# Performance work log

Hardware: AMD Instinct MI355X
Metric: run time of the kernel (lower is better)

## Reference

```python
import jax, jax.numpy as jnp
import numpy as np

N_CODES = 4096
DIM = 1280
N_TOKENS = 32768


def _l2norm(v, axis=-1, eps=1e-12):
    return v / jnp.maximum(jnp.linalg.norm(v, axis=axis, keepdims=True), eps)


def setup_inputs() -> dict:
    key = jax.random.key(0)
    kx, ke = jax.random.split(key)
    # inputs are L2-normalized vectors per the module's docstring
    x = _l2norm(jax.random.normal(kx, (N_TOKENS, DIM), dtype=jnp.float32))
    # codebook init: uniform(-1/n_codes, 1/n_codes) then L2-normalized (as in __init__)
    embed = jax.random.uniform(ke, (N_CODES, DIM), dtype=jnp.float32,
                               minval=-1.0 / N_CODES, maxval=1.0 / N_CODES)
    embed = _l2norm(embed)
    return {"x": x, "embed": embed}


def reference(x, embed):
    x_sq = jnp.sum(x * x, axis=1, keepdims=True)            # (N, 1)
    e_sq = jnp.sum(embed * embed, axis=1)[None, :]          # (1, K)
    dist = -(x_sq - 2.0 * (x @ embed.T) + e_sq)             # (N, K)
    indices = jnp.argmax(dist, axis=-1)                     # (N,)
    quantized = embed[indices]                              # gather (N, D)
    commit_loss = jnp.mean((x - quantized) ** 2)
    # straight-through estimator
    quantized_ste = x + jax.lax.stop_gradient(quantized - x)
    return quantized_ste, indices, commit_loss
```

## Files before the change

### kernel.cpp

```cpp
#include <hip/hip_runtime.h>
#include <hip/hip_bf16.h>

typedef int i32x4 __attribute__((ext_vector_type(4)));

#define N_TOKENS 32768
#define N_CODES 4096
#define DIM 1280
#define NT 20
#define BUFSZ 24576
#define NBUF 3

__device__ __forceinline__ void load_lds16(const void* g, void* l) {
    __builtin_amdgcn_global_load_lds(
        (const __attribute__((address_space(1))) unsigned int*)g,
        (__attribute__((address_space(3))) unsigned int*)l,
        16, 0, 0);
}

__global__ __launch_bounds__(256) void quantize_i8_kernel(
    const float* __restrict__ X, const float* __restrict__ E,
    signed char* __restrict__ Xq, signed char* __restrict__ Eq,
    float* __restrict__ sxs, float* __restrict__ ses)
{
    int row = blockIdx.x * 4 + (threadIdx.x >> 6);
    const float* src;
    signed char* dst;
    float* scale;
    if (row < N_TOKENS) {
        src = X + (size_t)row * DIM; dst = Xq + (size_t)row * DIM; scale = sxs + row;
    } else {
        int r = row - N_TOKENS;
        if (r >= N_CODES) return;
        src = E + (size_t)r * DIM; dst = Eq + (size_t)r * DIM; scale = ses + r;
    }
    int lane = threadIdx.x & 63;
    const float4* s4 = (const float4*)src;
    float4 v[5];
    float amax = 0.f;
    #pragma unroll
    for (int j = 0; j < 5; ++j) {
        v[j] = s4[j * 64 + lane];
        amax = fmaxf(amax, fmaxf(fmaxf(fabsf(v[j].x), fabsf(v[j].y)),
                                 fmaxf(fabsf(v[j].z), fabsf(v[j].w))));
    }
    #pragma unroll
    for (int d = 1; d < 64; d <<= 1) amax = fmaxf(amax, __shfl_xor(amax, d));
    amax = fmaxf(amax, 1e-20f);
    float inv = 127.0f / amax;
    int* d4 = (int*)dst;
    #pragma unroll
    for (int j = 0; j < 5; ++j) {
        int q0 = (int)rintf(v[j].x * inv), q1 = (int)rintf(v[j].y * inv);
        int q2 = (int)rintf(v[j].z * inv), q3 = (int)rintf(v[j].w * inv);
        d4[j * 64 + lane] = (q0 & 0xFF) | ((q1 & 0xFF) << 8) |
                            ((q2 & 0xFF) << 16) | ((q3 & 0xFF) << 24);
    }
    if (lane == 0) *scale = amax * (1.0f / 127.0f);
}

__global__ __launch_bounds__(512, 4) void gemm_argmax_kernel(
    const signed char* __restrict__ Xq, const signed char* __restrict__ Eq,
    const float* __restrict__ sx, const float* __restrict__ se,
    unsigned* __restrict__ pkeys)
{
    __shared__ __align__(16) char lds[NBUF * BUFSZ];

    int bid = blockIdx.x;
    int swz = (bid & 7) * 512 + (bid >> 3);
    int cb = swz >> 8, rb = swz & 255;
    int row0 = rb << 7, col0 = cb << 8;

    int tid = threadIdx.x;
    int wid = tid >> 6, lane = tid & 63;
    int wm = wid >> 2, wn = wid & 3;
    int lr = lane & 15, g = lane >> 4;

    int slot = (((lr & 1) << 2) + g) ^ ((lr >> 1) & 7);
    int aoff = ((wm << 5) + (lr >> 1)) * 128 + slot * 16;
    int boff = 8192 + ((wn << 5) + (lr >> 1)) * 128 + slot * 16;

    i32x4 acc[4][4] = {};

    auto STAGE = [&](int t) {
        int base = (t % NBUF) * BUFSZ;
        int k0 = t << 6;
        {
            int rp = tid >> 3, c = tid & 7;
            int cp = c ^ (rp & 7);
            int gr = (rp << 1) + (cp >> 2);
            int kc = k0 + ((cp & 3) << 4);
            load_lds16(Xq + (size_t)(row0 + gr) * DIM + kc, lds + base + (tid << 4));
        }
        #pragma unroll
        for (int i = 0; i < 2; ++i) {
            int f = tid + (i << 9);
            int rp = f >> 3, c = f & 7;
            int cp = c ^ (rp & 7);
            int gr = (rp << 1) + (cp >> 2);
            int kc = k0 + ((cp & 3) << 4);
            load_lds16(Eq + (size_t)(col0 + gr) * DIM + kc, lds + base + 8192 + (f << 4));
        }
    };

    auto COMPUTE = [&](int t) {
        int base = (t % NBUF) * BUFSZ;
        const char* pA = lds + base + aoff;
        const char* pB = lds + base + boff;
        i32x4 a[4], b[4];
        #pragma unroll
        for (int m = 0; m < 4; ++m) a[m] = *(const i32x4*)(pA + (m << 10));
        #pragma unroll
        for (int n = 0; n < 4; ++n) b[n] = *(const i32x4*)(pB + (n << 10));
        __builtin_amdgcn_s_setprio(1);
        #pragma unroll
        for (int m = 0; m < 4; ++m)
            #pragma unroll
            for (int n = 0; n < 4; ++n)
                acc[m][n] = __builtin_amdgcn_mfma_i32_16x16x64_i8(
                    a[m], b[n], acc[m][n], 0, 0, 0);
        __builtin_amdgcn_s_setprio(0);
    };

    STAGE(0); STAGE(1);
    asm volatile("s_waitcnt vmcnt(3)" ::: "memory");
    __builtin_amdgcn_s_barrier();
    __builtin_amdgcn_sched_barrier(0);

    for (int t = 0; t < NT - 2; ++t) {
        STAGE(t + 2);
        COMPUTE(t);
        asm volatile("s_waitcnt vmcnt(3)" ::: "memory");
        __builtin_amdgcn_s_barrier();
        __builtin_amdgcn_sched_barrier(0);
    }
    COMPUTE(NT - 2);
    asm volatile("s_waitcnt vmcnt(0)" ::: "memory");
    __builtin_amdgcn_s_barrier();
    __builtin_amdgcn_sched_barrier(0);
    COMPUTE(NT - 1);
    __syncthreads();

    float se_l[4];
    #pragma unroll
    for (int n = 0; n < 4; ++n)
        se_l[n] = se[col0 + (wn << 6) + (n << 4) + lr];

    uint2* lk2 = (uint2*)lds;
    #pragma unroll
    for (int m = 0; m < 4; ++m) {
        #pragma unroll
        for (int r = 0; r < 4; ++r) {
            int row = (wm << 6) + (m << 4) + (g << 2) + r;
            float fx = sx[row0 + row];
            unsigned b1 = 0, b2 = 0;
            #pragma unroll
            for (int n = 0; n < 4; ++n) {
                float s = (float)acc[m][n][r] * (fx * se_l[n]);
                int cib = ((wn & 1) << 6) + (n << 4) + lr;
                unsigned u = __float_as_uint(s);
                u = (u & 0x80000000u) ? ~u : (u | 0x80000000u);
                unsigned key = (u & 0xFFFFFF80u) | (unsigned)(127 - cib);
                if (key > b1) { b2 = b1; b1 = key; }
                else if (key > b2) b2 = key;
            }
            #pragma unroll
            for (int d = 1; d < 16; d <<= 1) {
                unsigned o1 = __shfl_xor(b1, d), o2 = __shfl_xor(b2, d);
                if (o1 > b1) { b2 = (b1 > o2) ? b1 : o2; b1 = o1; }
                else if (o1 > b2) b2 = o1;
            }
            if (lr == 0) {
                uint2 v; v.x = b1; v.y = b2;
                lk2[(row << 2) + wn] = v;
            }
        }
    }
    __syncthreads();
    if (tid < 256) {
        int row = tid >> 1, h = tid & 1;
        uint2 p0 = lk2[(row << 2) + (h << 1)];
        uint2 p1 = lk2[(row << 2) + (h << 1) + 1];
        unsigned b1 = p0.x, b2 = p0.y;
        if (p1.x > b1) { b2 = (b1 > p1.y) ? b1 : p1.y; b1 = p1.x; }
        else if (p1.x > b2) b2 = p1.x;
        uint2 out; out.x = b1; out.y = b2;
        *(uint2*)&pkeys[((size_t)(row0 + row) << 6) + (((cb << 1) + h) << 1)] = out;
    }
}

__global__ __launch_bounds__(64) void refine_gather_kernel(
    const float* __restrict__ X, const float* __restrict__ E,
    const unsigned* __restrict__ pkeys, float* __restrict__ outq,
    float* __restrict__ outidx, float* __restrict__ sums)
{
    int token = blockIdx.x;
    int lane = threadIdx.x;
    unsigned k = pkeys[((size_t)token << 6) + lane];
    unsigned m = k & 0xFFFFFF80u;
    float s = __uint_as_float((m & 0x80000000u) ? (m & 0x7FFFFFFFu) : ~m);
    float smax = s;
    #pragma unroll
    for (int d = 1; d < 64; d <<= 1) smax = fmaxf(smax, __shfl_xor(smax, d));
    bool cand = s >= smax - 3e-3f;
    unsigned long long ball = __ballot(cand);

    const float4* x4 = (const float4*)(X + (size_t)token * DIM);
    float4 xv[5];
    #pragma unroll
    for (int j = 0; j < 5; ++j) xv[j] = x4[j * 64 + lane];

    double best_s = -1.0e300;
    int best_i = 0x7FFFFFFF;
    while (ball) {
        int src = __ffsll(ball) - 1;
        ball &= ball - 1;
        unsigned ck = __shfl(k, src);
        int cidx = ((src >> 1) << 7) + (127 - (int)(ck & 127u));
        const float4* e4 = (const float4*)(E + (size_t)cidx * DIM);
        double d = 0.0, ee = 0.0;
        #pragma unroll
        for (int j = 0; j < 5; ++j) {
            float4 ev = e4[j * 64 + lane];
            d += (double)xv[j].x * (double)ev.x + (double)xv[j].y * (double)ev.y
               + (double)xv[j].z * (double)ev.z + (double)xv[j].w * (double)ev.w;
            ee += (double)ev.x * (double)ev.x + (double)ev.y * (double)ev.y
                + (double)ev.z * (double)ev.z + (double)ev.w * (double)ev.w;
        }
        #pragma unroll
        for (int dd = 1; dd < 64; dd <<= 1) {
            d += __shfl_xor(d, dd);
            ee += __shfl_xor(ee, dd);
        }
        double sc = 2.0 * d - ee;
        if (sc > best_s || (sc == best_s && cidx < best_i)) { best_s = sc; best_i = cidx; }
    }

    const float4* e4 = (const float4*)(E + (size_t)best_i * DIM);
    float4* o4 = (float4*)(outq + (size_t)token * DIM);
    float local = 0.0f;
    #pragma unroll
    for (int j = 0; j < 5; ++j) {
        float4 q = e4[j * 64 + lane];
        o4[j * 64 + lane] = q;
        float dx = xv[j].x - q.x, dy = xv[j].y - q.y;
        float dz = xv[j].z - q.z, dw = xv[j].w - q.w;
        local += dx * dx + dy * dy + dz * dz + dw * dw;
    }
    #pragma unroll
    for (int d = 1; d < 64; d <<= 1) local += __shfl_xor(local, d);
    if (lane == 0) {
        sums[token] = local;
        outidx[token] = (float)best_i;
    }
}

__global__ __launch_bounds__(256) void loss_kernel(
    const float* __restrict__ sums, float* __restrict__ out_loss)
{
    __shared__ double red[256];
    int t = threadIdx.x;
    double s = 0.0;
    for (int i = t; i < N_TOKENS; i += 256) s += (double)sums[i];
    red[t] = s;
    __syncthreads();
    for (int off = 128; off > 0; off >>= 1) {
        if (t < off) red[t] += red[t + off];
        __syncthreads();
    }
    if (t == 0) out_loss[0] = (float)(red[0] / (double)((size_t)N_TOKENS * DIM));
}

extern "C" void kernel_launch(void* const* d_in, const int* in_sizes, int n_in,
                              void* d_out, int out_size, void* d_ws, size_t ws_size,
                              hipStream_t stream)
{
    const float* X = (const float*)d_in[0];
    const float* E = (const float*)d_in[1];

    float* outq = (float*)d_out;
    float* outidx = outq + (size_t)N_TOKENS * DIM;
    float* outloss = outidx + N_TOKENS;

    signed char* Xq = (signed char*)d_out;
    signed char* Eq = Xq + (size_t)N_TOKENS * DIM;
    float* sxs = (float*)(Eq + (size_t)N_CODES * DIM);
    float* ses = sxs + N_TOKENS;

    unsigned* pkeys = (unsigned*)d_ws;
    float* sums = (float*)((char*)d_ws + (size_t)N_TOKENS * 64 * sizeof(unsigned));

    quantize_i8_kernel<<<dim3((N_TOKENS + N_CODES) / 4), dim3(256), 0, stream>>>(
        X, E, Xq, Eq, sxs, ses);
    gemm_argmax_kernel<<<dim3(4096), dim3(512), 0, stream>>>(Xq, Eq, sxs, ses, pkeys);
    refine_gather_kernel<<<dim3(N_TOKENS), dim3(64), 0, stream>>>(X, E, pkeys, outq, outidx, sums);
    loss_kernel<<<dim3(1), dim3(256), 0, stream>>>(sums, outloss);
}
```

Baseline: 380.5 us.

## Enlarge GEMM tile to 256x256 with 128-deep K double-buffered LDS pipeline

The int8 GEMM+argmax kernel moves from 128x256 tiles with a 3-stage 64-deep K pipeline to 256x256 tiles that use 128-deep K stages in two 64KB LDS buffers. Staging loads are interleaved across four MFMA phases per iteration, and the A/B tiles get a new 64-byte row swizzle. The larger tile doubles per-wave accumulators to 8x4 and halves global/LDS traffic per MFMA. In exchange, occupancy drops to 2 blocks per CU, register pressure rises, and the grid is halved to 2048 blocks.

```diff
diff --git a/kernel.cpp b/kernel.cpp
--- a/kernel.cpp
+++ b/kernel.cpp
@@ -6,9 +6,7 @@
 #define N_TOKENS 32768
 #define N_CODES 4096
 #define DIM 1280
-#define NT 20
-#define BUFSZ 24576
-#define NBUF 3
+#define NT 10
 
 __device__ __forceinline__ void load_lds16(const void* g, void* l) {
     __builtin_amdgcn_global_load_lds(
@@ -58,86 +56,93 @@
     if (lane == 0) *scale = amax * (1.0f / 127.0f);
 }
 
-__global__ __launch_bounds__(512, 4) void gemm_argmax_kernel(
+__global__ __launch_bounds__(512, 2) void gemm_argmax_kernel(
     const signed char* __restrict__ Xq, const signed char* __restrict__ Eq,
     const float* __restrict__ sx, const float* __restrict__ se,
     unsigned* __restrict__ pkeys)
 {
-    __shared__ __align__(16) char lds[NBUF * BUFSZ];
+    __shared__ __align__(16) char lds[131072];
 
     int bid = blockIdx.x;
-    int swz = (bid & 7) * 512 + (bid >> 3);
-    int cb = swz >> 8, rb = swz & 255;
-    int row0 = rb << 7, col0 = cb << 8;
+    int swz = (bid & 7) * 256 + (bid >> 3);
+    int cb0 = swz >> 7, rb = swz & 127;
+    int row0 = rb << 8, col0 = cb0 << 8;
 
     int tid = threadIdx.x;
     int wid = tid >> 6, lane = tid & 63;
     int wm = wid >> 2, wn = wid & 3;
     int lr = lane & 15, g = lane >> 4;
 
-    int slot = (((lr & 1) << 2) + g) ^ ((lr >> 1) & 7);
-    int aoff = ((wm << 5) + (lr >> 1)) * 128 + slot * 16;
-    int boff = 8192 + ((wn << 5) + (lr >> 1)) * 128 + slot * 16;
-
-    i32x4 acc[4][4] = {};
-
-    auto STAGE = [&](int t) {
-        int base = (t % NBUF) * BUFSZ;
-        int k0 = t << 6;
-        {
-            int rp = tid >> 3, c = tid & 7;
-            int cp = c ^ (rp & 7);
-            int gr = (rp << 1) + (cp >> 2);
-            int kc = k0 + ((cp & 3) << 4);
-            load_lds16(Xq + (size_t)(row0 + gr) * DIM + kc, lds + base + (tid << 4));
-        }
-        #pragma unroll
-        for (int i = 0; i < 2; ++i) {
-            int f = tid + (i << 9);
-            int rp = f >> 3, c = f & 7;
-            int cp = c ^ (rp & 7);
-            int gr = (rp << 1) + (cp >> 2);
-            int kc = k0 + ((cp & 3) << 4);
-            load_lds16(Eq + (size_t)(col0 + gr) * DIM + kc, lds + base + 8192 + (f << 4));
+    int chunk = g ^ ((lr >> 1) & 3);
+    int aoff = ((wm << 7) + lr) * 64 + (chunk << 4);
+    int boff = 32768 + ((wn << 6) + lr) * 64 + (chunk << 4);
+
+    int f0 = tid, f1 = tid + 512;
+    int cp0 = ((f0 & 3) ^ ((f0 >> 3) & 3)) << 4;
+    int cp1 = ((f1 & 3) ^ ((f1 >> 3) & 3)) << 4;
+    const signed char* sA0 = Xq + (size_t)(row0 + (f0 >> 2)) * DIM + cp0;
+    const signed char* sA1 = Xq + (size_t)(row0 + (f1 >> 2)) * DIM + cp1;
+    const signed char* sB0 = Eq + (size_t)(col0 + (f0 >> 2)) * DIM + cp0;
+    const signed char* sB1 = Eq + (size_t)(col0 + (f1 >> 2)) * DIM + cp1;
+    int dA0 = f0 << 4, dA1 = f1 << 4;
+    int dB0 = 32768 + (f0 << 4), dB1 = 32768 + (f1 << 4);
+
+    i32x4 acc[8][4] = {};
+
+    auto STAGE = [&](int H, int part) {
+        int dbase = ((H >> 1) & 1) * 65536 + (H & 1) * 16384;
+        int goff = H << 6;
+        if (part == 0) {
+            load_lds16(sA0 + goff, lds + dbase + dA0);
+            load_lds16(sA1 + goff, lds + dbase + dA1);
+        } else {
+            load_lds16(sB0 + goff, lds + dbase + dB0);
+            load_lds16(sB1 + goff, lds + dbase + dB1);
         }
     };
 
-    auto COMPUTE = [&](int t) {
-        int base = (t % NBUF) * BUFSZ;
-        const char* pA = lds + base + aoff;
-        const char* pB = lds + base + boff;
-        i32x4 a[4], b[4];
-        #pragma unroll
-        for (int m = 0; m < 4; ++m) a[m] = *(const i32x4*)(pA + (m << 10));
-        #pragma unroll
-        for (int n = 0; n < 4; ++n) b[n] = *(const i32x4*)(pB + (n << 10));
-        __builtin_amdgcn_s_setprio(1);
-        #pragma unroll
-        for (int m = 0; m < 4; ++m)
-            #pragma unroll
-            for (int n = 0; n < 4; ++n)
-                acc[m][n] = __builtin_amdgcn_mfma_i32_16x16x64_i8(
-                    a[m], b[n], acc[m][n], 0, 0, 0);
-        __builtin_amdgcn_s_setprio(0);
-    };
-
-    STAGE(0); STAGE(1);
-    asm volatile("s_waitcnt vmcnt(3)" ::: "memory");
+    STAGE(0, 0); STAGE(0, 1); STAGE(1, 0); STAGE(1, 1); STAGE(2, 0); STAGE(2, 1);
+    asm volatile("s_waitcnt vmcnt(8)" ::: "memory");
     __builtin_amdgcn_s_barrier();
     __builtin_amdgcn_sched_barrier(0);
 
-    for (int t = 0; t < NT - 2; ++t) {
-        STAGE(t + 2);
-        COMPUTE(t);
-        asm volatile("s_waitcnt vmcnt(3)" ::: "memory");
-        __builtin_amdgcn_s_barrier();
-        __builtin_amdgcn_sched_barrier(0);
-    }
-    COMPUTE(NT - 2);
-    asm volatile("s_waitcnt vmcnt(0)" ::: "memory");
-    __builtin_amdgcn_s_barrier();
-    __builtin_amdgcn_sched_barrier(0);
-    COMPUTE(NT - 1);
+    i32x4 a[4], b[4];
+    for (int t = 0; t < NT; ++t) {
+        int bufb = (t & 1) * 65536;
+        #pragma unroll
+        for (int P = 0; P < 4; ++P) {
+            const int kk = P >> 1, mb = (P & 1) * 4;
+            const char* base = lds + bufb + kk * 16384;
+            if ((P & 1) == 0) {
+                #pragma unroll
+                for (int n = 0; n < 4; ++n)
+                    b[n] = *(const i32x4*)(base + boff + (n << 10));
+            }
+            #pragma unroll
+            for (int j = 0; j < 4; ++j)
+                a[j] = *(const i32x4*)(base + aoff + ((mb + j) << 10));
+            if (P < 2) { if (t <= 8) STAGE(2 * t + 3, P); }
+            else       { if (t <= 7) STAGE(2 * t + 4, P - 2); }
+            __builtin_amdgcn_s_barrier();
+            __builtin_amdgcn_s_setprio(1);
+            #pragma unroll
+            for (int j = 0; j < 4; ++j)
+                #pragma unroll
+                for (int n = 0; n < 4; ++n)
+                    acc[mb + j][n] = __builtin_amdgcn_mfma_i32_16x16x64_i8(
+                        a[j], b[n], acc[mb + j][n], 0, 0, 0);
+            __builtin_amdgcn_s_setprio(0);
+            if (P == 1) {
+                if (t <= 8) { asm volatile("s_waitcnt vmcnt(8)" ::: "memory"); }
+                else        { asm volatile("s_waitcnt vmcnt(0)" ::: "memory"); }
+            } else if (P == 3) {
+                if (t <= 7)      { asm volatile("s_waitcnt vmcnt(8)" ::: "memory"); }
+                else if (t == 8) { asm volatile("s_waitcnt vmcnt(4)" ::: "memory"); }
+            }
+            __builtin_amdgcn_s_barrier();
+            __builtin_amdgcn_sched_barrier(0);
+        }
+    }
     __syncthreads();
 
     float se_l[4];
@@ -147,10 +152,10 @@
 
     uint2* lk2 = (uint2*)lds;
     #pragma unroll
-    for (int m = 0; m < 4; ++m) {
+    for (int m = 0; m < 8; ++m) {
         #pragma unroll
         for (int r = 0; r < 4; ++r) {
-            int row = (wm << 6) + (m << 4) + (g << 2) + r;
+            int row = (wm << 7) + (m << 4) + (g << 2) + r;
             float fx = sx[row0 + row];
             unsigned b1 = 0, b2 = 0;
             #pragma unroll
@@ -176,7 +181,7 @@
         }
     }
     __syncthreads();
-    if (tid < 256) {
+    {
         int row = tid >> 1, h = tid & 1;
         uint2 p0 = lk2[(row << 2) + (h << 1)];
         uint2 p1 = lk2[(row << 2) + (h << 1) + 1];
@@ -184,7 +189,7 @@
         if (p1.x > b1) { b2 = (b1 > p1.y) ? b1 : p1.y; b1 = p1.x; }
         else if (p1.x > b2) b2 = p1.x;
         uint2 out; out.x = b1; out.y = b2;
-        *(uint2*)&pkeys[((size_t)(row0 + row) << 6) + (((cb << 1) + h) << 1)] = out;
+        *(uint2*)&pkeys[((size_t)(row0 + row) << 6) + (((cb0 << 1) + h) << 1)] = out;
     }
 }
 
@@ -291,7 +296,7 @@
 
     quantize_i8_kernel<<<dim3((N_TOKENS + N_CODES) / 4), dim3(256), 0, stream>>>(
         X, E, Xq, Eq, sxs, ses);
-    gemm_argmax_kernel<<<dim3(4096), dim3(512), 0, stream>>>(Xq, Eq, sxs, ses, pkeys);
+    gemm_argmax_kernel<<<dim3(2048), dim3(512), 0, stream>>>(Xq, Eq, sxs, ses, pkeys);
     refine_gather_kernel<<<dim3(N_TOKENS), dim3(64), 0, stream>>>(X, E, pkeys, outq, outidx, sums);
     loss_kernel<<<dim3(1), dim3(256), 0, stream>>>(sums, outloss);
 }
```

After: 401.3 us. 1.05x slower.
